# Kernel tuning notes

Hardware: AMD Instinct MI355X
Metric: run time of the kernel (lower is better)

Reference implementation:

```python
import jax, jax.numpy as jnp
import numpy as np

DICT_LEN = 9
NUM_LS = 8
DIM = 1024
SEQ = 2048
BZ = 32


def setup_inputs() -> dict:
    key = jax.random.key(0)
    k_x, k_ids, k_w, k_b = jax.random.split(key, 4)
    x = jax.random.normal(k_x, (SEQ, BZ, DIM), dtype=jnp.float32)
    lang_ids = jax.random.randint(k_ids, (BZ,), 0, DICT_LEN)
    # torch nn.Linear init: U(-1/sqrt(in), 1/sqrt(in)), weight shape [out, in]
    bound = 1.0 / np.sqrt(DIM)
    W = jax.random.uniform(k_w, (NUM_LS, DIM, DIM), dtype=jnp.float32, minval=-bound, maxval=bound)
    b = jax.random.uniform(k_b, (NUM_LS, DIM), dtype=jnp.float32, minval=-bound, maxval=bound)
    return {"x": x, "lang_ids": lang_ids, "W": W, "b": b}


def reference(x, lang_ids, W, b):
    # Mapper.forward: gid = dict_len - 1 - lang_ids; tokens with gid in [1, num_ls]
    # are transformed by Linear #(gid-1); all other batch columns pass through.
    gid = DICT_LEN - 1 - lang_ids                      # [bz]
    active = (gid >= 1) & (gid <= NUM_LS)              # [bz]
    eidx = jnp.clip(gid - 1, 0, NUM_LS - 1)            # [bz] expert index (dummy 0 where inactive)
    We = W[eidx]                                       # [bz, dim, dim] (torch Linear weight layout [out, in])
    be = b[eidx]                                       # [bz, dim]
    y = jnp.einsum("sbd,bed->sbe", x, We) + be[None, :, :]
    return jnp.where(active[None, :, None], y, x)
```

## Files before the change

### kernel.cpp

```cpp
#include <hip/hip_runtime.h>
#include <hip/hip_bf16.h>

#define TSEQ 2048
#define TBZ  32
#define TDIM 1024
#define NLS  8

typedef __attribute__((ext_vector_type(8))) short bf16x8;
typedef __attribute__((ext_vector_type(4))) float f32x4;

__device__ inline unsigned int pk2(float lo, float hi) {
    __hip_bfloat162 h = __float22bfloat162_rn(make_float2(lo, hi));
    return *reinterpret_cast<const unsigned int*>(&h);
}

__device__ inline void gload_lds16(const void* g, void* l) {
    __builtin_amdgcn_global_load_lds(
        (const __attribute__((address_space(1))) unsigned int*)g,
        (__attribute__((address_space(3))) unsigned int*)l,
        16, 0, 0);
}

__global__ __launch_bounds__(256) void conv_all(
    const float* __restrict__ x, const int* __restrict__ lang_ids,
    const float* __restrict__ W,
    unsigned short* __restrict__ xb, unsigned short* __restrict__ wb,
    float* __restrict__ out)
{
    const int bid = blockIdx.x;
    if (bid < 512) {
        const int total = NLS * TDIM * TDIM / 8;
        const int stride = 512 * 256;
        for (int i = bid * 256 + threadIdx.x; i < total; i += stride) {
            const float* src = W + (long)i * 8;
            f32x4 v0 = *(const f32x4*)(src);
            f32x4 v1 = *(const f32x4*)(src + 4);
            uint4 o;
            o.x = pk2(v0.x, v0.y); o.y = pk2(v0.z, v0.w);
            o.z = pk2(v1.x, v1.y); o.w = pk2(v1.z, v1.w);
            *(uint4*)(wb + (long)i * 8) = o;
        }
        return;
    }
    const int xbid = bid - 512;
    const int total = TSEQ * TBZ * TDIM / 8;
    const int stride = 4096 * 256;
    for (int i = xbid * 256 + threadIdx.x; i < total; i += stride) {
        const int d8  = i & (TDIM / 8 - 1);
        const int row = i >> 7;
        const int b   = row & (TBZ - 1);
        const int gid = 8 - lang_ids[b];
        const float* src = x + (long)row * TDIM + d8 * 8;
        f32x4 v0 = *(const f32x4*)(src);
        f32x4 v1 = *(const f32x4*)(src + 4);
        if (gid >= 1 && gid <= 8) {
            const int s = row >> 5;
            uint4 o;
            o.x = pk2(v0.x, v0.y); o.y = pk2(v0.z, v0.w);
            o.z = pk2(v1.x, v1.y); o.w = pk2(v1.z, v1.w);
            *(uint4*)(xb + (long)(b * TSEQ + s) * TDIM + d8 * 8) = o;
        } else {
            float* dst = out + (long)row * TDIM + d8 * 8;
            *(f32x4*)(dst)     = v0;
            *(f32x4*)(dst + 4) = v1;
        }
    }
}


#define BAR __builtin_amdgcn_s_barrier()
#define LGKM asm volatile("s_waitcnt lgkmcnt(0)" ::: "memory")
#define VMC(n) asm volatile("s_waitcnt vmcnt(" #n ")" ::: "memory")
#define KAo(kv) (((kv) & 1023) + (((kv) >> 10) << 18))
#define KBo(kv) ((kv) & 1023)

__global__ __launch_bounds__(512, 2) void mapper_gemm8p(
    const unsigned short* __restrict__ xb,
    const int* __restrict__ lang_ids,
    const unsigned short* __restrict__ wb,
    const float* __restrict__ bias,
    float* __restrict__ out)
{
    const int p  = blockIdx.x;
    const int l  = (p & 7) * 64 + (p >> 3);
    const int b  = l >> 4;
    const int strip = (l >> 2) & 3;
    const int nt = l & 3;
    const int s0 = strip * 512;
    const int e0 = nt * 256;
    const int tid = threadIdx.x;

    const int gid = 8 - lang_ids[b];
    if (!(gid >= 1 && gid <= 8)) return;
    const int eb = gid - 1;

    __shared__ uint4 ldsbuf[131072 / 16];
    char* ldsc = (char*)ldsbuf;

    const int lane = tid & 63;
    const int wave = tid >> 6;
    const int wr   = wave >> 2;
    const int wc   = wave & 3;
    const int fr   = lane & 15;
    const int fq   = lane >> 4;
    const int fr7  = fr & 7;

    const unsigned short* __restrict__ Aab = xb + (long)b  * TSEQ * TDIM + (long)s0 * TDIM;
    const unsigned short* __restrict__ Bbb = wb + (long)eb * TDIM * TDIM + (long)e0 * TDIM;

    const int L    = lane;
    const int lch8 = ((L & 7) ^ (L >> 3)) * 8;
    const int ldA0 = wave * 2048 + L * 16;
    const unsigned short* aG[2][2];
    const unsigned short* bG[2][2];
    #pragma unroll
    for (int j = 0; j < 2; ++j) {
        const int rr = wave * 16 + j * 8 + (L >> 3);
        #pragma unroll
        for (int mh = 0; mh < 2; ++mh)
            aG[j][mh] = Aab + ((rr >> 6) * 128 + mh * 64 + (rr & 63)) * TDIM + lch8;
        #pragma unroll
        for (int nh = 0; nh < 2; ++nh)
            bG[j][nh] = Bbb + ((rr >> 5) * 64 + nh * 32 + (rr & 31)) * TDIM + lch8;
    }

#define STAGE_A(slot, mh, kofs) do { \
    gload_lds16(aG[0][mh] + (kofs), ldsc + (slot)*32768 + (mh)*16384 + ldA0); \
    gload_lds16(aG[1][mh] + (kofs), ldsc + (slot)*32768 + (mh)*16384 + ldA0 + 1024); \
} while (0)
#define STAGE_B(slot, nh, kofs) do { \
    gload_lds16(bG[0][nh] + (kofs), ldsc + 65536 + (slot)*32768 + (nh)*16384 + ldA0); \
    gload_lds16(bG[1][nh] + (kofs), ldsc + 65536 + (slot)*32768 + (nh)*16384 + ldA0 + 1024); \
} while (0)
#define RD_A(slot, mh) do { \
    _Pragma("unroll") for (int ml = 0; ml < 4; ++ml) { \
        const int rr = wr * 64 + ml * 16 + fr; \
        _Pragma("unroll") for (int kk = 0; kk < 2; ++kk) \
            af[ml][kk] = *(const bf16x8*)(ldsc + (slot)*32768 + (mh)*16384 + rr*128 + (((kk*4+fq) ^ fr7) << 4)); \
    } } while (0)
#define RD_B(slot, nh, br) do { \
    _Pragma("unroll") for (int nl = 0; nl < 2; ++nl) { \
        const int rr = wc * 32 + nl * 16 + fr; \
        _Pragma("unroll") for (int kk = 0; kk < 2; ++kk) \
            br[nl][kk] = *(const bf16x8*)(ldsc + 65536 + (slot)*32768 + (nh)*16384 + rr*128 + (((kk*4+fq) ^ fr7) << 4)); \
    } } while (0)
#define MM(mh, nh, br) do { \
    __builtin_amdgcn_s_setprio(1); \
    _Pragma("unroll") for (int ml = 0; ml < 4; ++ml) \
    _Pragma("unroll") for (int nl = 0; nl < 2; ++nl) \
    _Pragma("unroll") for (int kk = 0; kk < 2; ++kk) \
        acc[(mh)*4+ml][(nh)*2+nl] = __builtin_amdgcn_mfma_f32_16x16x32_bf16( \
            af[ml][kk], br[nl][kk], acc[(mh)*4+ml][(nh)*2+nl], 0, 0, 0); \
    __builtin_amdgcn_s_setprio(0); \
} while (0)

    f32x4 acc[8][4];
    #pragma unroll
    for (int m = 0; m < 8; ++m)
        #pragma unroll
        for (int n = 0; n < 4; ++n)
            acc[m][n] = (f32x4){0.f, 0.f, 0.f, 0.f};

    bf16x8 af[4][2], bf0[2][2], bf1[2][2];

    STAGE_A(0, 0, 0);  STAGE_B(0, 0, 0);  STAGE_B(0, 1, 0);  STAGE_A(0, 1, 0);
    STAGE_A(1, 0, 64); STAGE_B(1, 0, 64); STAGE_B(1, 1, 64);
    VMC(6); BAR;

    const int cr = lane >> 4;
    const int cc = lane & 15;

    for (int mtl = 0; mtl < 2; ++mtl) {
        for (int it = 0; it < 8; ++it) {
            const int kva = mtl * 1024 + it * 128;
            const int kb = kva + 64;
            const int kn = kva + 128;
            const int km = kva + 192;
            RD_A(0, 0); RD_B(0, 0, bf0); STAGE_A(1, 1, KAo(kb));
            BAR; LGKM; MM(0, 0, bf0); BAR;
            RD_B(0, 1, bf1); STAGE_A(0, 0, KAo(kn));
            BAR; LGKM; MM(0, 1, bf1); BAR;
            RD_A(0, 1); STAGE_B(0, 0, KBo(kn));
            BAR; LGKM; MM(1, 0, bf0); BAR;
            STAGE_B(0, 1, KBo(kn));
            BAR; MM(1, 1, bf1); VMC(6); BAR;
            RD_A(1, 0); RD_B(1, 0, bf0); STAGE_A(0, 1, KAo(kn));
            BAR; LGKM; MM(0, 0, bf0); BAR;
            RD_B(1, 1, bf1); STAGE_A(1, 0, KAo(km));
            BAR; LGKM; MM(0, 1, bf1); BAR;
            RD_A(1, 1); STAGE_B(1, 0, KBo(km));
            BAR; LGKM; MM(1, 0, bf0); BAR;
            STAGE_B(1, 1, KBo(km));
            BAR; MM(1, 1, bf1); VMC(6); BAR;
        }

        const int sb = s0 + mtl * 256 + wr * 128;
        #pragma unroll
        for (int n = 0; n < 4; ++n) {
            const int e  = e0 + wc * 64 + n * 16 + cc;
            const float bv = bias[eb * TDIM + e];
            #pragma unroll
            for (int m = 0; m < 8; ++m) {
                #pragma unroll
                for (int j = 0; j < 4; ++j) {
                    const int s = sb + m * 16 + cr * 4 + j;
                    out[(long)s * (TBZ * TDIM) + b * TDIM + e] = acc[m][n][j] + bv;
                }
            }
        }
        #pragma unroll
        for (int m = 0; m < 8; ++m)
            #pragma unroll
            for (int n = 0; n < 4; ++n)
                acc[m][n] = (f32x4){0.f, 0.f, 0.f, 0.f};
    }
#undef STAGE_A
#undef STAGE_B
#undef RD_A
#undef RD_B
#undef MM
}

__device__ inline unsigned short f2bf(float f) {
    union { float f; unsigned int u; } v; v.f = f;
    unsigned int r = v.u + 0x7fffu + ((v.u >> 16) & 1u);
    return (unsigned short)(r >> 16);
}
constexpr int FLDS = 40;

__global__ __launch_bounds__(256) void mapper_fused(
    const float* __restrict__ x, const int* __restrict__ lang_ids,
    const float* __restrict__ W, const float* __restrict__ bias,
    float* __restrict__ out)
{
    const int bid = blockIdx.x;
    const int b   = bid >> 7;
    const int t   = bid & 127;
    const int mt  = t >> 3;
    const int nt  = t & 7;
    const int s0  = mt * 128;
    const int e0  = nt * 128;
    const int tid = threadIdx.x;

    const int gid = 8 - lang_ids[b];
    const bool active = (gid >= 1) && (gid <= 8);
    int eb = gid - 1; eb = eb < 0 ? 0 : (eb > 7 ? 7 : eb);

    if (!active) {
        const f32x4* xs = (const f32x4*)x;
        f32x4*       os = (f32x4*)out;
        const int rs4 = TBZ * TDIM / 4;
        for (int i = tid; i < 128 * 128 / 4; i += 256) {
            int r = i >> 5, c = i & 31;
            long idx = (long)(s0 + r) * rs4 + b * (TDIM / 4) + (e0 >> 2) + c;
            os[idx] = xs[idx];
        }
        return;
    }

    __shared__ unsigned short As[128 * FLDS];
    __shared__ unsigned short Bs[128 * FLDS];
    const float* __restrict__ Wb = W + (long)eb * TDIM * TDIM;

    const int lane = tid & 63;
    const int wave = tid >> 6;
    const int wrr  = wave >> 1;
    const int wcc  = wave & 1;

    f32x4 acc[4][4];
    #pragma unroll
    for (int m = 0; m < 4; ++m)
        #pragma unroll
        for (int n = 0; n < 4; ++n)
            acc[m][n] = (f32x4){0.f, 0.f, 0.f, 0.f};

    const int rg = tid >> 3;
    const int cg = tid & 7;
    const int fr = lane & 15;
    const int fo = (lane >> 4) * 8;

    for (int k0 = 0; k0 < TDIM; k0 += 32) {
        __syncthreads();
        #pragma unroll
        for (int pp = 0; pp < 4; ++pp) {
            const int r = rg + pp * 32;
            f32x4 av = *(const f32x4*)(x  + (long)(s0 + r) * (TBZ * TDIM) + b * TDIM + k0 + cg * 4);
            f32x4 bv = *(const f32x4*)(Wb + (long)(e0 + r) * TDIM + k0 + cg * 4);
            unsigned int alo = (unsigned)f2bf(av.x) | ((unsigned)f2bf(av.y) << 16);
            unsigned int ahi = (unsigned)f2bf(av.z) | ((unsigned)f2bf(av.w) << 16);
            unsigned int blo = (unsigned)f2bf(bv.x) | ((unsigned)f2bf(bv.y) << 16);
            unsigned int bhi = (unsigned)f2bf(bv.z) | ((unsigned)f2bf(bv.w) << 16);
            *(uint2*)&As[r * FLDS + cg * 4] = make_uint2(alo, ahi);
            *(uint2*)&Bs[r * FLDS + cg * 4] = make_uint2(blo, bhi);
        }
        __syncthreads();

        bf16x8 af2[4], bfm[4];
        #pragma unroll
        for (int m = 0; m < 4; ++m)
            af2[m] = *(const bf16x8*)&As[(wrr * 64 + m * 16 + fr) * FLDS + fo];
        #pragma unroll
        for (int n = 0; n < 4; ++n)
            bfm[n] = *(const bf16x8*)&Bs[(wcc * 64 + n * 16 + fr) * FLDS + fo];
        #pragma unroll
        for (int m = 0; m < 4; ++m)
            #pragma unroll
            for (int n = 0; n < 4; ++n)
                acc[m][n] = __builtin_amdgcn_mfma_f32_16x16x32_bf16(af2[m], bfm[n], acc[m][n], 0, 0, 0);
    }

    const int cr = lane >> 4;
    const int cc = lane & 15;
    #pragma unroll
    for (int n = 0; n < 4; ++n) {
        const int e  = e0 + wcc * 64 + n * 16 + cc;
        const float bv = bias[eb * TDIM + e];
        #pragma unroll
        for (int m = 0; m < 4; ++m) {
            #pragma unroll
            for (int j = 0; j < 4; ++j) {
                const int s = s0 + wrr * 64 + m * 16 + cr * 4 + j;
                out[(long)s * (TBZ * TDIM) + b * TDIM + e] = acc[m][n][j] + bv;
            }
        }
    }
}

extern "C" void kernel_launch(void* const* d_in, const int* in_sizes, int n_in,
                              void* d_out, int out_size, void* d_ws, size_t ws_size,
                              hipStream_t stream) {
    const float* x        = (const float*)d_in[0];
    const int*   lang_ids = (const int*)d_in[1];
    const float* W        = (const float*)d_in[2];
    const float* bias     = (const float*)d_in[3];
    float*       out      = (float*)d_out;

    const size_t xbytes = (size_t)TSEQ * TBZ * TDIM * 2;
    const size_t wbytes = (size_t)NLS * TDIM * TDIM * 2;

    if (ws_size >= xbytes + wbytes) {
        unsigned short* xbp = (unsigned short*)d_ws;
        unsigned short* wbp = (unsigned short*)((char*)d_ws + xbytes);
        conv_all<<<4608, 256, 0, stream>>>(x, lang_ids, W, xbp, wbp, out);
        mapper_gemm8p<<<512, 512, 0, stream>>>(xbp, lang_ids, wbp, bias, out);
    } else {
        mapper_fused<<<TBZ * 16 * 8, 256, 0, stream>>>(x, lang_ids, W, bias, out);
    }
}
```

Measured before the change: 271.4 us.

## Swap MFMA operands for vectorized stores, move passthrough copy into GEMM kernel

The MFMA operand order is swapped so each lane's accumulator holds four consecutive output features. The epilogue can then write 16-byte float4 stores with a vector bias load instead of scalar strided stores. The copy of inactive batch columns moves from the conversion kernel into the GEMM kernel's early-exit path. However, conv_x now converts every column to bf16, including ones it no longer needs to. The weight conversion is split into its own launch, which adds one kernel launch.

```diff
diff --git a/kernel.cpp b/kernel.cpp
--- a/kernel.cpp
+++ b/kernel.cpp
@@ -21,49 +21,37 @@
         16, 0, 0);
 }
 
-__global__ __launch_bounds__(256) void conv_all(
-    const float* __restrict__ x, const int* __restrict__ lang_ids,
-    const float* __restrict__ W,
-    unsigned short* __restrict__ xb, unsigned short* __restrict__ wb,
-    float* __restrict__ out)
-{
-    const int bid = blockIdx.x;
-    if (bid < 512) {
-        const int total = NLS * TDIM * TDIM / 8;
-        const int stride = 512 * 256;
-        for (int i = bid * 256 + threadIdx.x; i < total; i += stride) {
-            const float* src = W + (long)i * 8;
-            f32x4 v0 = *(const f32x4*)(src);
-            f32x4 v1 = *(const f32x4*)(src + 4);
-            uint4 o;
-            o.x = pk2(v0.x, v0.y); o.y = pk2(v0.z, v0.w);
-            o.z = pk2(v1.x, v1.y); o.w = pk2(v1.z, v1.w);
-            *(uint4*)(wb + (long)i * 8) = o;
-        }
-        return;
-    }
-    const int xbid = bid - 512;
+__global__ __launch_bounds__(256) void conv_x(const float* __restrict__ x,
+                                              unsigned short* __restrict__ xb) {
     const int total = TSEQ * TBZ * TDIM / 8;
-    const int stride = 4096 * 256;
-    for (int i = xbid * 256 + threadIdx.x; i < total; i += stride) {
+    const int stride = gridDim.x * 256;
+    for (int i = blockIdx.x * 256 + threadIdx.x; i < total; i += stride) {
         const int d8  = i & (TDIM / 8 - 1);
         const int row = i >> 7;
+        const int s   = row >> 5;
         const int b   = row & (TBZ - 1);
-        const int gid = 8 - lang_ids[b];
         const float* src = x + (long)row * TDIM + d8 * 8;
         f32x4 v0 = *(const f32x4*)(src);
         f32x4 v1 = *(const f32x4*)(src + 4);
-        if (gid >= 1 && gid <= 8) {
-            const int s = row >> 5;
-            uint4 o;
-            o.x = pk2(v0.x, v0.y); o.y = pk2(v0.z, v0.w);
-            o.z = pk2(v1.x, v1.y); o.w = pk2(v1.z, v1.w);
-            *(uint4*)(xb + (long)(b * TSEQ + s) * TDIM + d8 * 8) = o;
-        } else {
-            float* dst = out + (long)row * TDIM + d8 * 8;
-            *(f32x4*)(dst)     = v0;
-            *(f32x4*)(dst + 4) = v1;
-        }
+        uint4 o;
+        o.x = pk2(v0.x, v0.y); o.y = pk2(v0.z, v0.w);
+        o.z = pk2(v1.x, v1.y); o.w = pk2(v1.z, v1.w);
+        *(uint4*)(xb + (long)(b * TSEQ + s) * TDIM + d8 * 8) = o;
+    }
+}
+
+__global__ __launch_bounds__(256) void conv_w(const float* __restrict__ W,
+                                              unsigned short* __restrict__ wb) {
+    const int total = NLS * TDIM * TDIM / 8;
+    const int stride = gridDim.x * 256;
+    for (int i = blockIdx.x * 256 + threadIdx.x; i < total; i += stride) {
+        const float* src = W + (long)i * 8;
+        f32x4 v0 = *(const f32x4*)(src);
+        f32x4 v1 = *(const f32x4*)(src + 4);
+        uint4 o;
+        o.x = pk2(v0.x, v0.y); o.y = pk2(v0.z, v0.w);
+        o.z = pk2(v1.x, v1.y); o.w = pk2(v1.z, v1.w);
+        *(uint4*)(wb + (long)i * 8) = o;
     }
 }
 
@@ -79,6 +67,7 @@
     const int* __restrict__ lang_ids,
     const unsigned short* __restrict__ wb,
     const float* __restrict__ bias,
+    const float* __restrict__ x,
     float* __restrict__ out)
 {
     const int p  = blockIdx.x;
@@ -91,7 +80,18 @@
     const int tid = threadIdx.x;
 
     const int gid = 8 - lang_ids[b];
-    if (!(gid >= 1 && gid <= 8)) return;
+    if (!(gid >= 1 && gid <= 8)) {
+        const f32x4* xs = (const f32x4*)x;
+        f32x4*       os = (f32x4*)out;
+        const int rs4 = TBZ * TDIM / 4;
+        for (int i = tid; i < 512 * 256 / 4; i += 512) {
+            int r = i >> 6;
+            int c = i & 63;
+            long idx = (long)(s0 + r) * rs4 + b * (TDIM / 4) + (e0 >> 2) + c;
+            os[idx] = xs[idx];
+        }
+        return;
+    }
     const int eb = gid - 1;
 
     __shared__ uint4 ldsbuf[131072 / 16];
@@ -150,7 +150,7 @@
     _Pragma("unroll") for (int nl = 0; nl < 2; ++nl) \
     _Pragma("unroll") for (int kk = 0; kk < 2; ++kk) \
         acc[(mh)*4+ml][(nh)*2+nl] = __builtin_amdgcn_mfma_f32_16x16x32_bf16( \
-            af[ml][kk], br[nl][kk], acc[(mh)*4+ml][(nh)*2+nl], 0, 0, 0); \
+            br[nl][kk], af[ml][kk], acc[(mh)*4+ml][(nh)*2+nl], 0, 0, 0); \
     __builtin_amdgcn_s_setprio(0); \
 } while (0)
 
@@ -167,8 +167,8 @@
     STAGE_A(1, 0, 64); STAGE_B(1, 0, 64); STAGE_B(1, 1, 64);
     VMC(6); BAR;
 
-    const int cr = lane >> 4;
-    const int cc = lane & 15;
+    const int cs  = lane & 15;
+    const int eqb = (lane >> 4) << 2;
 
     for (int mtl = 0; mtl < 2; ++mtl) {
         for (int it = 0; it < 8; ++it) {
@@ -197,15 +197,12 @@
         const int sb = s0 + mtl * 256 + wr * 128;
         #pragma unroll
         for (int n = 0; n < 4; ++n) {
-            const int e  = e0 + wc * 64 + n * 16 + cc;
-            const float bv = bias[eb * TDIM + e];
+            const int e = e0 + wc * 64 + n * 16 + eqb;
+            const f32x4 bv4 = *(const f32x4*)&bias[eb * TDIM + e];
             #pragma unroll
             for (int m = 0; m < 8; ++m) {
-                #pragma unroll
-                for (int j = 0; j < 4; ++j) {
-                    const int s = sb + m * 16 + cr * 4 + j;
-                    out[(long)s * (TBZ * TDIM) + b * TDIM + e] = acc[m][n][j] + bv;
-                }
+                const int s = sb + m * 16 + cs;
+                *(f32x4*)&out[(long)s * (TBZ * TDIM) + b * TDIM + e] = acc[m][n] + bv4;
             }
         }
         #pragma unroll
@@ -310,10 +307,10 @@
     }
 
     const int cr = lane >> 4;
-    const int cc = lane & 15;
+    const int cc2 = lane & 15;
     #pragma unroll
     for (int n = 0; n < 4; ++n) {
-        const int e  = e0 + wcc * 64 + n * 16 + cc;
+        const int e  = e0 + wcc * 64 + n * 16 + cc2;
         const float bv = bias[eb * TDIM + e];
         #pragma unroll
         for (int m = 0; m < 4; ++m) {
@@ -341,8 +338,9 @@
     if (ws_size >= xbytes + wbytes) {
         unsigned short* xbp = (unsigned short*)d_ws;
         unsigned short* wbp = (unsigned short*)((char*)d_ws + xbytes);
-        conv_all<<<4608, 256, 0, stream>>>(x, lang_ids, W, xbp, wbp, out);
-        mapper_gemm8p<<<512, 512, 0, stream>>>(xbp, lang_ids, wbp, bias, out);
+        conv_x<<<4096, 256, 0, stream>>>(x, xbp);
+        conv_w<<<2048, 256, 0, stream>>>(W, wbp);
+        mapper_gemm8p<<<512, 512, 0, stream>>>(xbp, lang_ids, wbp, bias, x, out);
     } else {
         mapper_fused<<<TBZ * 16 * 8, 256, 0, stream>>>(x, lang_ids, W, bias, out);
     }
```

New measurement: 260.4 us. 4.0% less time.
